# Performance work log

Hardware: AMD Instinct MI355X
Metric: run time of the kernel (lower is better)

## Reference

```python
import jax, jax.numpy as jnp
import numpy as np


def setup_inputs() -> dict:
    key = jax.random.key(0)
    k0, k1, k2, k3 = jax.random.split(key, 4)
    B, H, W, C, h = 2, 64, 64, 256, 8
    N = H * W
    # per-pixel, per-head (dy, dx) match offsets; a few pixels of displacement
    max_offset = jax.random.normal(k0, (B, N, h, 2), dtype=jnp.float32) * 4.0
    q = jax.random.normal(k1, (B, N, C), dtype=jnp.float32)
    k = jax.random.normal(k2, (B, N, C), dtype=jnp.float32)
    v = jax.random.normal(k3, (B, N, C), dtype=jnp.float32)
    return {"max_offset": max_offset, "q": q, "k": k, "v": v,
            "H": H, "W": W, "r_h": 3, "r_w": 3}


def reference(max_offset, q, k, v, H, W, r_h, r_w):
    """MatchAttention fused forward (l1_norm, scale=1.0).

    Each query pixel (y,x), head g attends to a (2*r_h+1)x(2*r_w+1) window
    centered at (y,x) + round(max_offset[...,g]), clamped to the image.
    Similarity is the negative L1 distance between q and gathered k.
    Returns (output [B,N,C], attn_out [B,N,h,K]).
    """
    B, N, C = q.shape
    h = max_offset.shape[2]
    Ch = C // h
    scale = 1.0
    attn_type = "l1_norm"  # fixed; 'l2_norm' would use squared distance

    # window deltas, K = (2*r_h+1)*(2*r_w+1)
    dy = jnp.arange(-r_h, r_h + 1)
    dx = jnp.arange(-r_w, r_w + 1)
    gy, gx = jnp.meshgrid(dy, dx, indexing="ij")
    ddy, ddx = gy.reshape(-1), gx.reshape(-1)  # [K]

    ys = (jnp.arange(N) // W)[None, :, None]  # [1,N,1]
    xs = (jnp.arange(N) % W)[None, :, None]

    off = jnp.round(max_offset).astype(jnp.int32)  # [B,N,h,2] (dy,dx)
    cy = ys + off[..., 0]                          # [B,N,h] window center
    cx = xs + off[..., 1]
    py = jnp.clip(cy[..., None] + ddy, 0, H - 1)   # [B,N,h,K]
    px = jnp.clip(cx[..., None] + ddx, 0, W - 1)
    idx = py * W + px                              # flat pixel index, [B,N,h,K]

    # split heads and move head axis forward: [B,h,N,Ch]
    qh = q.reshape(B, N, h, Ch).transpose(0, 2, 1, 3)
    kh = k.reshape(B, N, h, Ch).transpose(0, 2, 1, 3)
    vh = v.reshape(B, N, h, Ch).transpose(0, 2, 1, 3)
    idx_t = idx.transpose(0, 2, 1, 3)              # [B,h,N,K]

    # gather windows: [B,h,N,K,Ch]
    gather = jax.vmap(jax.vmap(lambda tbl, i: tbl[i]))
    kg = gather(kh, idx_t)
    vg = gather(vh, idx_t)

    # negative L1 distance similarity, softmax over window
    sim = -scale * jnp.abs(qh[:, :, :, None, :] - kg).sum(-1)  # [B,h,N,K]
    attn = jax.nn.softmax(sim, axis=-1)

    out = jnp.einsum("bhnk,bhnkc->bhnc", attn, vg)
    output = out.transpose(0, 2, 1, 3).reshape(B, N, C)
    attn_out = attn.transpose(0, 2, 1, 3)          # [B,N,h,K]
    return output, attn_out
```

## Files before the change

kernel.cpp:

```cpp
#include <hip/hip_runtime.h>
#include <hip/hip_fp16.h>
#include <math.h>

constexpr int B = 2, H = 64, W = 64, C = 256, NH = 8, CH = 32;
constexpr int R = 3, KW = 7, KK = 49, N = H * W;
constexpr int PIX = 32;
constexpr float LOG2E = 1.4426950408889634f;

typedef _Float16 h16x2 __attribute__((ext_vector_type(2)));

template <int CTRL>
static __device__ __forceinline__ float dpp_mov(float v) {
  union { float f; int i; } u;
  u.f = v;
  u.i = __builtin_amdgcn_update_dpp(u.i, u.i, CTRL, 0xf, 0xf, true);
  return u.f;
}
#define DPP_QUAD_XOR1 0xB1
#define DPP_QUAD_XOR2 0x4E
#define DPP_HALF_MIRROR 0x141

static __device__ __forceinline__ h16x2 h2n(__half2 x) {
  union { __half2 h; h16x2 n; } u;
  u.h = x;
  return u.n;
}

__global__ void __launch_bounds__(256) pack_kv_kernel(
    const float* __restrict__ kp, const float* __restrict__ vp,
    __half* __restrict__ kv) {
  const int idx = blockIdx.x * 256 + threadIdx.x;
  const int e8 = idx & 7;
  const int g = (idx >> 3) & 7;
  const int bn = idx >> 6;
  const int b = bn >> 12;
  const int n = bn & (N - 1);
  const float4 kf = *(const float4*)(kp + (size_t)bn * C + g * CH + e8 * 4);
  const float4 vf = *(const float4*)(vp + (size_t)bn * C + g * CH + e8 * 4);
  __half2 o[4];
  o[0] = __floats2half2_rn(kf.x * LOG2E, kf.y * LOG2E);
  o[1] = __floats2half2_rn(kf.z * LOG2E, kf.w * LOG2E);
  o[2] = __floats2half2_rn(vf.x, vf.y);
  o[3] = __floats2half2_rn(vf.z, vf.w);
  *(float4*)(kv + (((size_t)(b * NH + g) * N + n) * 64 + e8 * 8)) = *(float4*)o;
}

union KV { float4 f; __half2 h[4]; h16x2 n[4]; };

__global__ void __launch_bounds__(256, 2) match_attn_kernel(
    const float* __restrict__ moff, const float* __restrict__ qp,
    const __half* __restrict__ kvp, float* __restrict__ outp,
    float* __restrict__ attnp) {
  const int t = threadIdx.x;
  const int e8 = t & 7;
  const int p = t >> 3;

  const int xcd = blockIdx.x & 7;
  const int rest = blockIdx.x >> 3;
  const int bg = xcd * 2 + (rest >> 7);
  const int slot = rest & 127;
  const int y = slot >> 1;
  const int x = (slot & 1) * PIX + p;
  const int g = bg & 7;
  const int b = bg >> 3;
  const int n = y * W + x;

  const float2 off = *(const float2*)(moff + ((size_t)(b * N + n) * NH + g) * 2);
  const int cy = y + (int)rintf(off.x);
  const int cx = x + (int)rintf(off.y);

  int pxo[KW];
#pragma unroll
  for (int i = 0; i < KW; ++i) pxo[i] = min(max(cx + i - R, 0), W - 1) << 7;
  const char* __restrict__ kvb =
      (const char*)kvp + (size_t)(b * NH + g) * N * 128;
  const int lane16 = e8 * 16;

  const int chn = g * CH + e8 * 4;
  const float4 q0 = *(const float4*)(qp + (size_t)(b * N + n) * C + chn);
  const __half2 q01 = __floats2half2_rn(q0.x * LOG2E, q0.y * LOG2E);
  const __half2 q23 = __floats2half2_rn(q0.z * LOG2E, q0.w * LOG2E);
  const h16x2 one2 = {(_Float16)1.0f, (_Float16)1.0f};

  float ev7[KW];
#pragma unroll
  for (int i = 0; i < KW; ++i) ev7[i] = 0.f;
  float4 acc = {0.f, 0.f, 0.f, 0.f};
  float d0 = 0.f, d1 = 0.f;

#define ROWBASE(iy) ((min(max(cy + (iy)-R, 0), H - 1) << 13) + lane16)
#define LOADROW(buf, iy)                                      \
  {                                                           \
    const int _rb = ROWBASE(iy);                              \
    _Pragma("unroll") for (int ix = 0; ix < KW; ++ix)         \
        buf[ix].f = *(const float4*)(kvb + (_rb + pxo[ix]));  \
  }
#define COMPROW(buf, iy)                                                     \
  {                                                                          \
    const bool _own = ((iy) == e8);                                          \
    _Pragma("unroll") for (int ix = 0; ix < KW; ++ix) {                      \
      const h16x2 d01 = h2n(__habs2(__hsub2(q01, buf[ix].h[0])));            \
      const h16x2 d23 = h2n(__habs2(__hsub2(q23, buf[ix].h[1])));            \
      float s = __builtin_amdgcn_fdot2(                                      \
          d01, one2, __builtin_amdgcn_fdot2(d23, one2, 0.0f, false), false); \
      s += dpp_mov<DPP_QUAD_XOR1>(s);                                        \
      s += dpp_mov<DPP_QUAD_XOR2>(s);                                        \
      s += dpp_mov<DPP_HALF_MIRROR>(s);                                      \
      const float e = __builtin_amdgcn_exp2f(-s);  \
      if (ix & 1) d1 += e; else d0 += e;                                     \
      if (_own) ev7[ix] = e;                                                 \
      const h16x2 v01 = buf[ix].n[2], v23 = buf[ix].n[3];                    \
      acc.x = fmaf(e, (float)v01.x, acc.x);                                  \
      acc.y = fmaf(e, (float)v01.y, acc.y);                                  \
      acc.z = fmaf(e, (float)v23.x, acc.z);                                  \
      acc.w = fmaf(e, (float)v23.y, acc.w);                                  \
    }                                                                        \
  }

  KV A[KW], Bf[KW];
  LOADROW(A, 0)
#pragma clang loop unroll(disable)
  for (int ty = 0; ty < KW - 1; ty += 2) {
    LOADROW(Bf, ty + 1)
    COMPROW(A, ty)
    LOADROW(A, ty + 2)
    COMPROW(Bf, ty + 1)
  }
  COMPROW(A, KW - 1)

  const float inv = 1.0f / (d0 + d1);
  float4 o;
  o.x = acc.x * inv; o.y = acc.y * inv; o.z = acc.z * inv; o.w = acc.w * inv;
  *(float4*)(outp + (size_t)(b * N + n) * C + chn) = o;

  if (e8 < KW) {
    float* attn_row = attnp + ((size_t)(b * N + n) * NH + g) * KK + e8 * KW;
#pragma unroll
    for (int ix = 0; ix < KW; ++ix) attn_row[ix] = ev7[ix] * inv;
  }
}

extern "C" void kernel_launch(void* const* d_in, const int* in_sizes, int n_in,
                              void* d_out, int out_size, void* d_ws, size_t ws_size,
                              hipStream_t stream) {
  const float* moff = (const float*)d_in[0];
  const float* q    = (const float*)d_in[1];
  const float* k    = (const float*)d_in[2];
  const float* v    = (const float*)d_in[3];
  float* out  = (float*)d_out;
  float* attn = out + (size_t)B * N * C;
  __half* kv = (__half*)d_ws;

  pack_kv_kernel<<<B * N * NH * 8 / 256, 256, 0, stream>>>(k, v, kv);
  const int grid = B * NH * N / PIX;
  match_attn_kernel<<<grid, 256, 0, stream>>>(moff, q, kv, out, attn);
}
```

Before: 110.1 us.

## Stage KV window rows into LDS via async global_load_lds double buffering

```diff
diff --git a/kernel.cpp b/kernel.cpp
--- a/kernel.cpp
+++ b/kernel.cpp
@@ -26,6 +26,12 @@
   return u.n;
 }
 
+static __device__ __forceinline__ void gload_lds16(const void* g, void* l) {
+  __builtin_amdgcn_global_load_lds(
+      (const __attribute__((address_space(1))) void*)g,
+      (__attribute__((address_space(3))) void*)l, 16, 0, 0);
+}
+
 __global__ void __launch_bounds__(256) pack_kv_kernel(
     const float* __restrict__ kp, const float* __restrict__ vp,
     __half* __restrict__ kv) {
@@ -52,8 +58,11 @@
     const __half* __restrict__ kvp, float* __restrict__ outp,
     float* __restrict__ attnp) {
   const int t = threadIdx.x;
+  const int lane = t & 63;
   const int e8 = t & 7;
   const int p = t >> 3;
+  const int wid = t >> 6;
+  const int phm = p & 7;
 
   const int xcd = blockIdx.x & 7;
   const int rest = blockIdx.x >> 3;
@@ -69,12 +78,27 @@
   const int cy = y + (int)rintf(off.x);
   const int cx = x + (int)rintf(off.y);
 
-  int pxo[KW];
+  const int sy = min(max(cy - R, 0), H - KW);
+  const int sx = min(max(cx - R, 0), W - KW);
+
+  int cofs[KW], ryv[KW];
 #pragma unroll
-  for (int i = 0; i < KW; ++i) pxo[i] = min(max(cx + i - R, 0), W - 1) << 7;
+  for (int i = 0; i < KW; ++i) {
+    cofs[i] = (min(max(cx + i - R, 0), W - 1) - sx) * 8;
+    ryv[i] = min(max(cy + i - R, 0), H - 1) - sy;
+  }
+  const int rye8 = min(max(cy + e8 - R, 0), H - 1) - sy;
+
   const char* __restrict__ kvb =
       (const char*)kvp + (size_t)(b * NH + g) * N * 128;
-  const int lane16 = e8 * 16;
+  const int syxb = sy * 8192 + sx * 128;
+  const int laneoff = min(lane * 16, 880);
+  const char* vb[8];
+#pragma unroll
+  for (int ph = 0; ph < 8; ++ph)
+    vb[ph] = kvb + (__shfl(syxb, ph * 8) + laneoff);
+
+  __shared__ KV slots[4][2][8][64];
 
   const int chn = g * CH + e8 * 4;
   const float4 q0 = *(const float4*)(qp + (size_t)(b * N + n) * C + chn);
@@ -88,45 +112,48 @@
   float4 acc = {0.f, 0.f, 0.f, 0.f};
   float d0 = 0.f, d1 = 0.f;
 
-#define ROWBASE(iy) ((min(max(cy + (iy)-R, 0), H - 1) << 13) + lane16)
-#define LOADROW(buf, iy)                                      \
-  {                                                           \
-    const int _rb = ROWBASE(iy);                              \
-    _Pragma("unroll") for (int ix = 0; ix < KW; ++ix)         \
-        buf[ix].f = *(const float4*)(kvb + (_rb + pxo[ix]));  \
-  }
-#define COMPROW(buf, iy)                                                     \
+#define ISSUE(r, bf)                                             \
+  { _Pragma("unroll") for (int ph = 0; ph < 8; ++ph)             \
+        gload_lds16(vb[ph] + (r) * 8192, &slots[wid][bf][ph][0]); }
+#define LGKM0 asm volatile("s_waitcnt lgkmcnt(0)" ::: "memory");
+#define WAITV8 asm volatile("s_waitcnt vmcnt(8)" ::: "memory");
+#define WAITV0 asm volatile("s_waitcnt vmcnt(0)" ::: "memory");
+
+#define COMPROW(rr, bf)                                                      \
   {                                                                          \
-    const bool _own = ((iy) == e8);                                          \
+    float mr = 0.f;                                                          \
+    _Pragma("unroll") for (int iy = 0; iy < KW; ++iy)                        \
+        mr += (ryv[iy] == (rr)) ? 1.f : 0.f;                                 \
+    const bool _own = (rye8 == (rr));                                        \
     _Pragma("unroll") for (int ix = 0; ix < KW; ++ix) {                      \
-      const h16x2 d01 = h2n(__habs2(__hsub2(q01, buf[ix].h[0])));            \
-      const h16x2 d23 = h2n(__habs2(__hsub2(q23, buf[ix].h[1])));            \
+      KV kvv = slots[wid][bf][phm][cofs[ix] + e8];                           \
+      const h16x2 d01 = h2n(__habs2(__hsub2(q01, kvv.h[0])));                \
+      const h16x2 d23 = h2n(__habs2(__hsub2(q23, kvv.h[1])));                \
       float s = __builtin_amdgcn_fdot2(                                      \
           d01, one2, __builtin_amdgcn_fdot2(d23, one2, 0.0f, false), false); \
       s += dpp_mov<DPP_QUAD_XOR1>(s);                                        \
       s += dpp_mov<DPP_QUAD_XOR2>(s);                                        \
       s += dpp_mov<DPP_HALF_MIRROR>(s);                                      \
       const float e = __builtin_amdgcn_exp2f(-s);  \
-      if (ix & 1) d1 += e; else d0 += e;                                     \
+      const float em = e * mr;                                               \
+      if (ix & 1) d1 += em; else d0 += em;                                   \
       if (_own) ev7[ix] = e;                                                 \
-      const h16x2 v01 = buf[ix].n[2], v23 = buf[ix].n[3];                    \
-      acc.x = fmaf(e, (float)v01.x, acc.x);                                  \
-      acc.y = fmaf(e, (float)v01.y, acc.y);                                  \
-      acc.z = fmaf(e, (float)v23.x, acc.z);                                  \
-      acc.w = fmaf(e, (float)v23.y, acc.w);                                  \
+      const h16x2 v01 = kvv.n[2], v23 = kvv.n[3];                            \
+      acc.x = fmaf(em, (float)v01.x, acc.x);                                 \
+      acc.y = fmaf(em, (float)v01.y, acc.y);                                 \
+      acc.z = fmaf(em, (float)v23.x, acc.z);                                 \
+      acc.w = fmaf(em, (float)v23.y, acc.w);                                 \
     }                                                                        \
   }
 
-  KV A[KW], Bf[KW];
-  LOADROW(A, 0)
-#pragma clang loop unroll(disable)
-  for (int ty = 0; ty < KW - 1; ty += 2) {
-    LOADROW(Bf, ty + 1)
-    COMPROW(A, ty)
-    LOADROW(A, ty + 2)
-    COMPROW(Bf, ty + 1)
-  }
-  COMPROW(A, KW - 1)
+  ISSUE(0, 0)
+  ISSUE(1, 1) WAITV8 COMPROW(0, 0)
+  LGKM0 ISSUE(2, 0) WAITV8 COMPROW(1, 1)
+  LGKM0 ISSUE(3, 1) WAITV8 COMPROW(2, 0)
+  LGKM0 ISSUE(4, 0) WAITV8 COMPROW(3, 1)
+  LGKM0 ISSUE(5, 1) WAITV8 COMPROW(4, 0)
+  LGKM0 ISSUE(6, 0) WAITV8 COMPROW(5, 1)
+  WAITV0 COMPROW(6, 0)
 
   const float inv = 1.0f / (d0 + d1);
   float4 o;
```

Measured after the change: 120.2 us. 1.09x slower.
